# Kernel optimization log

Hardware: AMD Instinct MI355X
Metric: run time of the kernel (lower is better)

Reference implementation:

```python
import jax, jax.numpy as jnp
import numpy as np

NEG_BIG = -9.0e15  # matches -9000000000000000.0 fill in the torch code


def setup_inputs() -> dict:
    key = jax.random.key(0)
    ks = jax.random.split(key, 8)
    N, Fin, Fout = 8192, 256, 128
    input = jax.random.normal(ks[0], (N, Fin), dtype=jnp.float32)
    adj = jax.random.randint(ks[1], (N, N), 0, 2, dtype=jnp.int32)
    s_fc = 1.0 / np.sqrt(Fin)
    s_at = 1.0 / np.sqrt(Fout)
    W_fc = jax.random.normal(ks[2], (Fin, Fout), dtype=jnp.float32) * s_fc
    b_fc = jax.random.normal(ks[3], (Fout,), dtype=jnp.float32) * s_fc
    w_ax = jax.random.normal(ks[4], (Fout, 1), dtype=jnp.float32) * s_at
    b_ax = jax.random.normal(ks[5], (1,), dtype=jnp.float32) * s_at
    w_an = jax.random.normal(ks[6], (Fout, 1), dtype=jnp.float32) * s_at
    b_an = jax.random.normal(ks[7], (1,), dtype=jnp.float32) * s_at
    return {"input": input, "adj": adj, "W_fc": W_fc, "b_fc": b_fc,
            "w_ax": w_ax, "b_ax": b_ax, "w_an": w_an, "b_an": b_an}


def reference(input, adj, W_fc, b_fc, w_ax, b_ax, w_an, b_an):
    # x = fc(input): [N, Fout]
    x = input @ W_fc + b_fc
    # rank-1 additive scores: att_x(x) [N,1] + att_nei(x).T [1,N] -> [N,N]
    x_att = x @ w_ax + b_ax          # [N, 1]
    neib_att = (x @ w_an + b_an).T   # [1, N]
    ws = x_att + neib_att            # [N, N]
    # adjacency mask + row softmax
    ws = jnp.where(adj > 0, ws, NEG_BIG)
    ws = jax.nn.softmax(ws, axis=1)
    # dense aggregation + residual + ELU (dropout is identity in eval)
    out = jax.nn.elu(x + ws @ x)
    return out
```

## Files before the change

### kernel.cpp

```cpp
#include <hip/hip_runtime.h>
#include <hip/hip_bf16.h>
#include <math.h>


using f32x4  = __attribute__((ext_vector_type(4))) float;
using bf16x8 = __attribute__((ext_vector_type(8))) short;

#define N_NODES 8192
#define FIN     256
#define FOUT    128
#define NPAD    144
#define NSPLIT  8
#define KCHUNK  (N_NODES / NSPLIT)

#define X_OFF    0u
#define T_OFF    (X_OFF + N_NODES*FOUT*4u)
#define PMAX_OFF (T_OFF + N_NODES*4u)
#define GMAX_OFF (PMAX_OFF + 1024u)
#define YT_OFF   (GMAX_OFF + 512u)
#define P_OFF    (YT_OFF + (size_t)NPAD*N_NODES*2u)

__device__ __forceinline__ unsigned short f2bf(float f) {
  unsigned int u = __float_as_uint(f);
  unsigned int r = (u + 0x7FFFu + ((u >> 16) & 1u)) >> 16;
  return (unsigned short)r;
}

__device__ __forceinline__ void gload_lds16(const void* gsrc, void* ldst) {
  __builtin_amdgcn_global_load_lds(
      (const __attribute__((address_space(1))) void*)gsrc,
      (__attribute__((address_space(3))) void*)ldst, 16, 0, 0);
}

__global__ __launch_bounds__(256) void k1_fc(const float* __restrict__ in,
    const float* __restrict__ Wfc, const float* __restrict__ bfc,
    float* __restrict__ x) {
  __shared__ float sm[16 * FIN];
  const int tid = threadIdx.x;
  const int r0  = blockIdx.x * 16;
  const float4* gin = reinterpret_cast<const float4*>(in + (size_t)r0 * FIN);
  float4* sm4 = reinterpret_cast<float4*>(sm);
  #pragma unroll
  for (int i = 0; i < 4; i++) sm4[i * 256 + tid] = gin[i * 256 + tid];
  __syncthreads();
  const int d = tid & 127, g = tid >> 7;
  const float bias = bfc[d];
  float acc[8];
  #pragma unroll
  for (int r = 0; r < 8; r++) acc[r] = bias;
  const float4* s4 = reinterpret_cast<const float4*>(sm);
  for (int k = 0; k < FIN; k += 4) {
    float w0 = Wfc[(k + 0) * FOUT + d];
    float w1 = Wfc[(k + 1) * FOUT + d];
    float w2 = Wfc[(k + 2) * FOUT + d];
    float w3 = Wfc[(k + 3) * FOUT + d];
    #pragma unroll
    for (int r = 0; r < 8; r++) {
      float4 iv = s4[((g * 8 + r) * FIN + k) >> 2];
      acc[r] = fmaf(iv.x, w0, acc[r]);
      acc[r] = fmaf(iv.y, w1, acc[r]);
      acc[r] = fmaf(iv.z, w2, acc[r]);
      acc[r] = fmaf(iv.w, w3, acc[r]);
    }
  }
  #pragma unroll
  for (int r = 0; r < 8; r++)
    x[(size_t)(r0 + g * 8 + r) * FOUT + d] = acc[r];
}

__global__ __launch_bounds__(256) void k2_att(const float* __restrict__ x,
    const float* __restrict__ wan, const float* __restrict__ ban,
    float* __restrict__ t, float* __restrict__ pmax) {
  __shared__ float wm[4];
  const int tid = threadIdx.x, lane = tid & 63, w = tid >> 6;
  const float w0 = wan[lane], w1 = wan[lane + 64];
  const float bb = ban[0];
  float tmax = -1e30f;
  const int rbase = blockIdx.x * 32 + w * 8;
  for (int rr = 0; rr < 8; rr++) {
    const int row = rbase + rr;
    float p = x[(size_t)row * FOUT + lane] * w0
            + x[(size_t)row * FOUT + 64 + lane] * w1;
    #pragma unroll
    for (int m = 1; m < 64; m <<= 1) p += __shfl_xor(p, m);
    const float tv = p + bb;
    if (lane == 0) t[row] = tv;
    tmax = fmaxf(tmax, tv);
  }
  if (lane == 0) wm[w] = tmax;
  __syncthreads();
  if (tid == 0)
    pmax[blockIdx.x] = fmaxf(fmaxf(wm[0], wm[1]), fmaxf(wm[2], wm[3]));
}

__global__ void k3_gmax(const float* __restrict__ pmax, float* __restrict__ gmax) {
  float v = fmaxf(fmaxf(pmax[threadIdx.x], pmax[threadIdx.x + 64]),
                  fmaxf(pmax[threadIdx.x + 128], pmax[threadIdx.x + 192]));
  #pragma unroll
  for (int m = 1; m < 64; m <<= 1) v = fmaxf(v, __shfl_xor(v, m));
  if (threadIdx.x == 0) gmax[0] = v;
}

__global__ __launch_bounds__(256) void k4_y(const float* __restrict__ x,
    const float* __restrict__ t, const float* __restrict__ gmax,
    unsigned short* __restrict__ Yf) {
  __shared__ unsigned short sm[NPAD * 64];
  const int tid = threadIdx.x, lane = tid & 63, w = tid >> 6;
  const int jj = lane, j = blockIdx.x * 64 + jj;
  const float e = expf(t[j] - gmax[0]);
  const float4* x4 = reinterpret_cast<const float4*>(x + (size_t)j * FOUT + w * 32);
  #pragma unroll
  for (int dd = 0; dd < 8; dd++) {
    float4 xv = x4[dd];
    const int c = w * 32 + dd * 4;
    sm[(c + 0) * 64 + jj] = f2bf(e * xv.x);
    sm[(c + 1) * 64 + jj] = f2bf(e * xv.y);
    sm[(c + 2) * 64 + jj] = f2bf(e * xv.z);
    sm[(c + 3) * 64 + jj] = f2bf(e * xv.w);
  }
  #pragma unroll
  for (int i = 0; i < 4; i++) {
    const int c = 128 + w * 4 + i;
    sm[c * 64 + jj] = (c == 128) ? f2bf(e) : (unsigned short)0;
  }
  __syncthreads();
  for (int c5 = w; c5 < 18; c5 += 4) {
    const int wnd = c5 / 9, nf = c5 % 9;
    const int srcIdx = (nf * 16 + (lane & 15)) * 64 + wnd * 32 + (lane >> 4) * 8;
    bf16x8 v = *reinterpret_cast<const bf16x8*>(&sm[srcIdx]);
    const size_t Wg = (size_t)blockIdx.x * 2 + wnd;
    *reinterpret_cast<bf16x8*>(Yf + (Wg * 9 + nf) * 512 + lane * 8) = v;
  }
}

__global__ __launch_bounds__(256) void k5_gemm(const int* __restrict__ adj,
    const unsigned short* __restrict__ Yf, float* __restrict__ P) {
  __shared__ int ldsA[2][64 * 64];
  const int tid  = threadIdx.x;
  const int lane = tid & 63, w = tid >> 6;
  const int bm = blockIdx.x, s = blockIdx.y;
  const int q  = lane >> 4;
  const int rsub = lane >> 4, cb16 = (lane & 15) << 4;
  const unsigned short* bbase = Yf + (size_t)s * 32 * 9 * 512 + lane * 8;

  f32x4 acc[9];
  #pragma unroll
  for (int nf = 0; nf < 9; nf++) acc[nf] = (f32x4){0.f, 0.f, 0.f, 0.f};

#define STAGE_A(kbase_, buf_) { \
    _Pragma("unroll") \
    for (int i = 0; i < 4; i++) { \
      const int rit = w * 16 + i * 4 + rsub; \
      const int gcb = cb16 ^ ((rit & 7) << 4); \
      const char* gsrc = (const char*)adj + (((size_t)(bm * 64 + rit)) << 15) \
                       + (size_t)(s * KCHUNK + (kbase_)) * 4 + gcb; \
      gload_lds16(gsrc, (char*)&ldsA[buf_][(w * 16 + i * 4) * 64]); \
    } }

#define LOAD_B(dst_, wnd_) { \
    const unsigned short* p_ = bbase + (size_t)(wnd_) * 9 * 512; \
    _Pragma("unroll") \
    for (int nf = 0; nf < 9; nf++) \
      dst_[nf] = *reinterpret_cast<const bf16x8*>(p_ + nf * 512); \
  }

#define AFRAG(buf_, kk_, a0_, a1_) { \
    const int r_ = lane & 15; \
    const int sw_ = (r_ & 7) << 4; \
    const char* rowb_ = (const char*)&ldsA[buf_][(w * 16 + r_) * 64]; \
    const int cb0_ = ((kk_) + q * 8) * 4; \
    a0_ = *reinterpret_cast<const int4*>(rowb_ + (cb0_ ^ sw_)); \
    a1_ = *reinterpret_cast<const int4*>(rowb_ + ((cb0_ + 16) ^ sw_)); \
  }

#define MFMA9(a0_, a1_, B_) { \
    union { bf16x8 v; unsigned int u[4]; } af; \
    af.u[0] = (unsigned int)((a0_).x | ((a0_).y << 16)) * 0x3F80u; \
    af.u[1] = (unsigned int)((a0_).z | ((a0_).w << 16)) * 0x3F80u; \
    af.u[2] = (unsigned int)((a1_).x | ((a1_).y << 16)) * 0x3F80u; \
    af.u[3] = (unsigned int)((a1_).z | ((a1_).w << 16)) * 0x3F80u; \
    _Pragma("unroll") \
    for (int nf = 0; nf < 9; nf++) \
      acc[nf] = __builtin_amdgcn_mfma_f32_16x16x32_bf16(af.v, B_[nf], acc[nf], 0, 0, 0); \
  }

  bf16x8 Be[9], Bo[9];
  int4 a0, a1;

  STAGE_A(0, 0);
  LOAD_B(Be, 0);
  LOAD_B(Bo, 1);
  __syncthreads();

  for (int t = 0; t < 16; ++t) {
    const int buf = t & 1;
    if (t < 15) STAGE_A((t + 1) * 64, buf ^ 1);
    AFRAG(buf, 0, a0, a1);
    MFMA9(a0, a1, Be);
    if (t < 15) LOAD_B(Be, 2 * t + 2);
    AFRAG(buf, 32, a0, a1);
    MFMA9(a0, a1, Bo);
    if (t < 15) LOAD_B(Bo, 2 * t + 3);
    __syncthreads();
  }
#undef STAGE_A
#undef LOAD_B
#undef AFRAG
#undef MFMA9

  float* Pp = P + (size_t)s * N_NODES * NPAD;
  const int colb = lane & 15;
  #pragma unroll
  for (int nf = 0; nf < 9; nf++) {
    if (nf == 8 && colb != 0) continue;
    #pragma unroll
    for (int r = 0; r < 4; r++) {
      const int grow = bm * 64 + w * 16 + q * 4 + r;
      Pp[(size_t)grow * NPAD + nf * 16 + colb] = acc[nf][r];
    }
  }
}

__global__ __launch_bounds__(256) void k6_fin(const float* __restrict__ P,
    const float* __restrict__ x, float* __restrict__ out) {
  const int gid = blockIdx.x * 256 + threadIdx.x;
  const int i = gid >> 7, d = gid & 127;
  const size_t base = (size_t)i * NPAD;
  float num = 0.f, Z = 0.f;
  #pragma unroll
  for (int s = 0; s < NSPLIT; s++) {
    num += P[(size_t)s * N_NODES * NPAD + base + d];
    Z   += P[(size_t)s * N_NODES * NPAD + base + 128];
  }
  const float agg = (Z > 0.f) ? num / Z : 0.f;
  const float v = x[(size_t)i * FOUT + d] + agg;
  out[gid] = (v > 0.f) ? v : expm1f(v);
}

extern "C" void kernel_launch(void* const* d_in, const int* in_sizes, int n_in,
                              void* d_out, int out_size, void* d_ws, size_t ws_size,
                              hipStream_t stream) {
  const float* input = (const float*)d_in[0];
  const int*   adj   = (const int*)d_in[1];
  const float* Wfc   = (const float*)d_in[2];
  const float* bfc   = (const float*)d_in[3];
  const float* wan   = (const float*)d_in[6];
  const float* ban   = (const float*)d_in[7];

  char* ws = (char*)d_ws;
  float*          x    = (float*)(ws + X_OFF);
  float*          t    = (float*)(ws + T_OFF);
  float*          pmax = (float*)(ws + PMAX_OFF);
  float*          gmax = (float*)(ws + GMAX_OFF);
  unsigned short* Yf   = (unsigned short*)(ws + YT_OFF);
  float*          P    = (float*)(ws + P_OFF);
  float*          out  = (float*)d_out;

  k1_fc  <<<dim3(512),         dim3(256), 0, stream>>>(input, Wfc, bfc, x);
  k2_att <<<dim3(256),         dim3(256), 0, stream>>>(x, wan, ban, t, pmax);
  k3_gmax<<<dim3(1),           dim3(64),  0, stream>>>(pmax, gmax);
  k4_y   <<<dim3(128),         dim3(256), 0, stream>>>(x, t, gmax, Yf);
  k5_gemm<<<dim3(128, NSPLIT), dim3(256), 0, stream>>>(adj, Yf, P);
  k6_fin <<<dim3(4096),        dim3(256), 0, stream>>>(P, x, out);
}
```

Before: 459.4 us.

## Pack adjacency into bitmasks before the masked aggregation GEMM

Adds a pre-pass kernel that reads the int32 adjacency matrix and uses wave ballots to compress each row into 64-bit masks. The GEMM kernel then reads these compact masks straight into registers and expands the bits into bf16 0/1 A-fragments. This removes the LDS staging, swizzled fragment loads and per-iteration barriers from the inner loop. The full adjacency is still streamed once, now by a separate kernel, which adds one launch and an 8 MB intermediate buffer.

```diff
diff --git a/kernel.cpp b/kernel.cpp
--- a/kernel.cpp
+++ b/kernel.cpp
@@ -19,6 +19,7 @@
 #define GMAX_OFF (PMAX_OFF + 1024u)
 #define YT_OFF   (GMAX_OFF + 512u)
 #define P_OFF    (YT_OFF + (size_t)NPAD*N_NODES*2u)
+#define ADJP_OFF (P_OFF + (size_t)NSPLIT*N_NODES*NPAD*4u)
 
 __device__ __forceinline__ unsigned short f2bf(float f) {
   unsigned int u = __float_as_uint(f);
@@ -26,10 +27,21 @@
   return (unsigned short)r;
 }
 
-__device__ __forceinline__ void gload_lds16(const void* gsrc, void* ldst) {
-  __builtin_amdgcn_global_load_lds(
-      (const __attribute__((address_space(1))) void*)gsrc,
-      (__attribute__((address_space(3))) void*)ldst, 16, 0, 0);
+__global__ __launch_bounds__(256) void k0_pack(const int* __restrict__ adj,
+    unsigned long long* __restrict__ adjP) {
+  const int lane = threadIdx.x & 63, w = threadIdx.x >> 6;
+  const int row = blockIdx.x * 4 + w;
+  const int* src = adj + (size_t)row * N_NODES;
+  unsigned long long mine = 0;
+  for (int h = 0; h < 2; ++h) {
+    #pragma unroll 16
+    for (int g = 0; g < 64; ++g) {
+      int v = src[h * 4096 + g * 64 + lane];
+      unsigned long long m = __ballot(v != 0);
+      if (lane == g) mine = m;
+    }
+    adjP[(size_t)row * 128 + h * 64 + lane] = mine;
+  }
 }
 
 __global__ __launch_bounds__(256) void k1_fc(const float* __restrict__ in,
@@ -133,29 +145,21 @@
   }
 }
 
-__global__ __launch_bounds__(256) void k5_gemm(const int* __restrict__ adj,
+__global__ __launch_bounds__(256) void k5_gemm(
+    const unsigned long long* __restrict__ adjP,
     const unsigned short* __restrict__ Yf, float* __restrict__ P) {
-  __shared__ int ldsA[2][64 * 64];
   const int tid  = threadIdx.x;
   const int lane = tid & 63, w = tid >> 6;
   const int bm = blockIdx.x, s = blockIdx.y;
-  const int q  = lane >> 4;
-  const int rsub = lane >> 4, cb16 = (lane & 15) << 4;
+  const int q  = lane >> 4, r = lane & 15;
+  const int row_g = bm * 64 + w * 16 + r;
+  const unsigned long long* ap = adjP + (size_t)row_g * 128 + s * 16;
   const unsigned short* bbase = Yf + (size_t)s * 32 * 9 * 512 + lane * 8;
+  const int qs = q * 8;
 
   f32x4 acc[9];
   #pragma unroll
   for (int nf = 0; nf < 9; nf++) acc[nf] = (f32x4){0.f, 0.f, 0.f, 0.f};
-
-#define STAGE_A(kbase_, buf_) { \
-    _Pragma("unroll") \
-    for (int i = 0; i < 4; i++) { \
-      const int rit = w * 16 + i * 4 + rsub; \
-      const int gcb = cb16 ^ ((rit & 7) << 4); \
-      const char* gsrc = (const char*)adj + (((size_t)(bm * 64 + rit)) << 15) \
-                       + (size_t)(s * KCHUNK + (kbase_)) * 4 + gcb; \
-      gload_lds16(gsrc, (char*)&ldsA[buf_][(w * 16 + i * 4) * 64]); \
-    } }
 
 #define LOAD_B(dst_, wnd_) { \
     const unsigned short* p_ = bbase + (size_t)(wnd_) * 9 * 512; \
@@ -164,49 +168,37 @@
       dst_[nf] = *reinterpret_cast<const bf16x8*>(p_ + nf * 512); \
   }
 
-#define AFRAG(buf_, kk_, a0_, a1_) { \
-    const int r_ = lane & 15; \
-    const int sw_ = (r_ & 7) << 4; \
-    const char* rowb_ = (const char*)&ldsA[buf_][(w * 16 + r_) * 64]; \
-    const int cb0_ = ((kk_) + q * 8) * 4; \
-    a0_ = *reinterpret_cast<const int4*>(rowb_ + (cb0_ ^ sw_)); \
-    a1_ = *reinterpret_cast<const int4*>(rowb_ + ((cb0_ + 16) ^ sw_)); \
-  }
-
-#define MFMA9(a0_, a1_, B_) { \
+#define MFMA_BITS(b_, B_) { \
     union { bf16x8 v; unsigned int u[4]; } af; \
-    af.u[0] = (unsigned int)((a0_).x | ((a0_).y << 16)) * 0x3F80u; \
-    af.u[1] = (unsigned int)((a0_).z | ((a0_).w << 16)) * 0x3F80u; \
-    af.u[2] = (unsigned int)((a1_).x | ((a1_).y << 16)) * 0x3F80u; \
-    af.u[3] = (unsigned int)((a1_).z | ((a1_).w << 16)) * 0x3F80u; \
+    _Pragma("unroll") \
+    for (int i2 = 0; i2 < 4; i2++) { \
+      const unsigned bq = (b_) >> (2 * i2); \
+      af.u[i2] = ((bq & 1u) ? 0x3F80u : 0u) | ((bq & 2u) ? 0x3F800000u : 0u); \
+    } \
     _Pragma("unroll") \
     for (int nf = 0; nf < 9; nf++) \
       acc[nf] = __builtin_amdgcn_mfma_f32_16x16x32_bf16(af.v, B_[nf], acc[nf], 0, 0, 0); \
   }
 
   bf16x8 Be[9], Bo[9];
-  int4 a0, a1;
-
-  STAGE_A(0, 0);
+  unsigned long long Ac = ap[0];
+  unsigned long long An = ap[1];
   LOAD_B(Be, 0);
   LOAD_B(Bo, 1);
-  __syncthreads();
 
   for (int t = 0; t < 16; ++t) {
-    const int buf = t & 1;
-    if (t < 15) STAGE_A((t + 1) * 64, buf ^ 1);
-    AFRAG(buf, 0, a0, a1);
-    MFMA9(a0, a1, Be);
+    const unsigned lo = (unsigned)Ac, hi = (unsigned)(Ac >> 32);
+    const unsigned be_ = (lo >> qs) & 0xFFu;
+    MFMA_BITS(be_, Be);
     if (t < 15) LOAD_B(Be, 2 * t + 2);
-    AFRAG(buf, 32, a0, a1);
-    MFMA9(a0, a1, Bo);
+    const unsigned bo_ = (hi >> qs) & 0xFFu;
+    MFMA_BITS(bo_, Bo);
     if (t < 15) LOAD_B(Bo, 2 * t + 3);
-    __syncthreads();
-  }
-#undef STAGE_A
+    Ac = An;
+    if (t < 14) An = ap[t + 2];
+  }
 #undef LOAD_B
-#undef AFRAG
-#undef MFMA9
+#undef MFMA_BITS
 
   float* Pp = P + (size_t)s * N_NODES * NPAD;
   const int colb = lane & 15;
@@ -214,9 +206,9 @@
   for (int nf = 0; nf < 9; nf++) {
     if (nf == 8 && colb != 0) continue;
     #pragma unroll
-    for (int r = 0; r < 4; r++) {
-      const int grow = bm * 64 + w * 16 + q * 4 + r;
-      Pp[(size_t)grow * NPAD + nf * 16 + colb] = acc[nf][r];
+    for (int rr = 0; rr < 4; rr++) {
+      const int grow = bm * 64 + w * 16 + q * 4 + rr;
+      Pp[(size_t)grow * NPAD + nf * 16 + colb] = acc[nf][rr];
     }
   }
 }
@@ -248,18 +240,20 @@
   const float* ban   = (const float*)d_in[7];
 
   char* ws = (char*)d_ws;
-  float*          x    = (float*)(ws + X_OFF);
-  float*          t    = (float*)(ws + T_OFF);
-  float*          pmax = (float*)(ws + PMAX_OFF);
-  float*          gmax = (float*)(ws + GMAX_OFF);
-  unsigned short* Yf   = (unsigned short*)(ws + YT_OFF);
-  float*          P    = (float*)(ws + P_OFF);
-  float*          out  = (float*)d_out;
-
+  float*              x    = (float*)(ws + X_OFF);
+  float*              t    = (float*)(ws + T_OFF);
+  float*              pmax = (float*)(ws + PMAX_OFF);
+  float*              gmax = (float*)(ws + GMAX_OFF);
+  unsigned short*     Yf   = (unsigned short*)(ws + YT_OFF);
+  float*              P    = (float*)(ws + P_OFF);
+  unsigned long long* adjP = (unsigned long long*)(ws + ADJP_OFF);
+  float*              out  = (float*)d_out;
+
+  k0_pack<<<dim3(2048),        dim3(256), 0, stream>>>(adj, adjP);
   k1_fc  <<<dim3(512),         dim3(256), 0, stream>>>(input, Wfc, bfc, x);
   k2_att <<<dim3(256),         dim3(256), 0, stream>>>(x, wan, ban, t, pmax);
   k3_gmax<<<dim3(1),           dim3(64),  0, stream>>>(pmax, gmax);
   k4_y   <<<dim3(128),         dim3(256), 0, stream>>>(x, t, gmax, Yf);
-  k5_gemm<<<dim3(128, NSPLIT), dim3(256), 0, stream>>>(adj, Yf, P);
+  k5_gemm<<<dim3(128, NSPLIT), dim3(256), 0, stream>>>(adjP, Yf, P);
   k6_fin <<<dim3(4096),        dim3(256), 0, stream>>>(P, x, out);
 }
```

After: 454.9 us. About the same (-1.0%).
